# Optimization experiments

Hardware: AMD Instinct MI355X
Metric: run time of the kernel (lower is better)

Reference implementation:

```python
import jax, jax.numpy as jnp
import numpy as np

N_MFS = 2
N_FEATURES = 12
OUTPUT_DIM = 8
BATCH = 4096
N_RULES = N_MFS ** N_FEATURES  # 4096


def _rule_indices(n_features, n_mfs):
    r = np.arange(n_mfs ** n_features)
    # mixed-radix digits: indices[rule, feat] = (rule // n_mfs**feat) % n_mfs
    return np.stack([(r // (n_mfs ** f)) % n_mfs for f in range(n_features)], axis=1).astype(np.int32)


def setup_inputs() -> dict:
    key = jax.random.key(0)
    ks = jax.random.split(key, 6)
    x = jax.random.normal(ks[0], (BATCH, N_FEATURES), dtype=jnp.float32)
    center_base = jax.random.uniform(ks[1], (N_FEATURES, 1), minval=-1.0, maxval=0.0, dtype=jnp.float32)
    center_delta_raw = jax.random.normal(ks[2], (N_FEATURES, N_MFS - 1), dtype=jnp.float32) * 0.5
    width_raw = jax.random.normal(ks[3], (N_FEATURES, N_MFS), dtype=jnp.float32) * 0.5
    fan = N_RULES * N_FEATURES + OUTPUT_DIM
    limit = float(np.sqrt(6.0 / fan))
    consequent_p = jax.random.uniform(ks[4], (N_RULES, N_FEATURES, OUTPUT_DIM), minval=-limit, maxval=limit, dtype=jnp.float32)
    consequent_r = jnp.zeros((N_RULES, OUTPUT_DIM), dtype=jnp.float32)
    rule_mf_indices = jnp.asarray(_rule_indices(N_FEATURES, N_MFS))
    return {"x": x, "center_base": center_base, "center_delta_raw": center_delta_raw,
            "width_raw": width_raw, "consequent_p": consequent_p, "consequent_r": consequent_r,
            "rule_mf_indices": rule_mf_indices}


def reference(x, center_base, center_delta_raw, width_raw, consequent_p, consequent_r, rule_mf_indices):
    # ordered centers: base + cumsum(softplus(delta) + 1e-3)
    gaps = jax.nn.softplus(center_delta_raw) + 1e-3          # (F, M-1)
    offsets = jnp.cumsum(gaps, axis=1)
    centers = jnp.concatenate([center_base, center_base + offsets], axis=1)  # (F, M)
    widths = jax.nn.softplus(width_raw) + 1e-3                # (F, M)

    # Gaussian memberships: (B, F, M)
    d = x[:, :, None] - centers[None, :, :]
    memberships = jnp.exp(-jnp.square(d) / (2.0 * jnp.square(widths)[None, :, :]))

    # rule firing: product over features of gathered memberships (loop over small fixed F)
    firing = jnp.ones((x.shape[0], rule_mf_indices.shape[0]), dtype=x.dtype)  # (B, R)
    for f in range(memberships.shape[1]):
        firing = firing * memberships[:, f, :][:, rule_mf_indices[:, f]]
    firing_norm = firing / (jnp.sum(firing, axis=1, keepdims=True) + 1e-8)

    # per-rule linear consequents: (B, R, O)
    rule_outputs = jnp.einsum('bf,rfo->bro', x, consequent_p) + consequent_r[None, :, :]
    # weighted reduce over rules: (B, O)
    output = jnp.einsum('br,bro->bo', firing_norm, rule_outputs)
    return output
```

## Files before the change

### kernel.cpp

```cpp
#include <hip/hip_runtime.h>
#include <math.h>

#define NF 12
#define NB 4096
#define NR 4096
#define NO 8

typedef float f32x4v __attribute__((ext_vector_type(4)));
typedef short bf16x8 __attribute__((ext_vector_type(8)));
typedef unsigned int uint32x4 __attribute__((ext_vector_type(4)));

#define PT2_BYTES (128 * 8 * 512 * 2)
#define PPART_OFF PT2_BYTES
#define PPART_BYTES (8 * NB * NO * 4)
#define WS_NEED (PT2_BYTES + PPART_BYTES)
#define PT_ELEMS (112 * 4096)

__device__ __forceinline__ float softplus_f(float v) {
    return fmaxf(v, 0.0f) + log1pf(__expf(-fabsf(v)));
}
__device__ __forceinline__ unsigned short f2bf(float f) {
    unsigned u = __float_as_uint(f);
    u += 0x7FFFu + ((u >> 16) & 1u);
    return (unsigned short)(u >> 16);
}
__device__ __forceinline__ unsigned cvt_pk_bf16(float a, float b) {
    unsigned r;
    asm("v_cvt_pk_bf16_f32 %0, %1, %2" : "=v"(r) : "v"(a), "v"(b));
    return r;
}

__device__ __forceinline__ void build_split(f32x4v va, f32x4v vb,
                                            bf16x8& ah, bf16x8& al) {
    unsigned h0 = cvt_pk_bf16(va[0], va[1]), h1 = cvt_pk_bf16(va[2], va[3]);
    unsigned h2 = cvt_pk_bf16(vb[0], vb[1]), h3 = cvt_pk_bf16(vb[2], vb[3]);
    f32x4v hia = { __uint_as_float(h0 << 16), __uint_as_float(h0 & 0xFFFF0000u),
                   __uint_as_float(h1 << 16), __uint_as_float(h1 & 0xFFFF0000u) };
    f32x4v hib = { __uint_as_float(h2 << 16), __uint_as_float(h2 & 0xFFFF0000u),
                   __uint_as_float(h3 << 16), __uint_as_float(h3 & 0xFFFF0000u) };
    f32x4v ea = va - hia;
    f32x4v eb = vb - hib;
    unsigned q0 = cvt_pk_bf16(ea[0], ea[1]), q1 = cvt_pk_bf16(ea[2], ea[3]);
    unsigned q2 = cvt_pk_bf16(eb[0], eb[1]), q3 = cvt_pk_bf16(eb[2], eb[3]);
    union { uint32x4 u; bf16x8 v; } A, B;
    A.u = (uint32x4){h0, h1, h2, h3};
    B.u = (uint32x4){q0, q1, q2, q3};
    ah = A.v; al = B.v;
}

__global__ __launch_bounds__(512) void anfis_prep3(
    const float* __restrict__ cp, const float* __restrict__ cr,
    unsigned short* __restrict__ PT2)
{
    __shared__ float s_cp[32 * 97];
    __shared__ float s_cr[32 * 8];
    const int kt = blockIdx.x;
    const int tid = threadIdx.x;

    {
        const float4* cp4 = (const float4*)(cp + (size_t)kt * 32 * 96);
        for (int i = tid; i < 768; i += 512) {
            float4 v = cp4[i];
            int r = i / 24, c4 = i - r * 24;
            float* d = &s_cp[r * 97 + c4 * 4];
            d[0] = v.x; d[1] = v.y; d[2] = v.z; d[3] = v.w;
        }
        if (tid < 64) {
            float4 v = ((const float4*)(cr + (size_t)kt * 32 * 8))[tid];
            float* d = &s_cr[tid * 4];
            d[0] = v.x; d[1] = v.y; d[2] = v.z; d[3] = v.w;
        }
    }
    __syncthreads();

    const int g = tid >> 7, col = (tid >> 3) & 15, e = tid & 7;
    const int rr = g * 8 + e;
    #pragma unroll
    for (int j = 0; j < 8; ++j) {
        int n = j * 16 + col;
        float v = 0.f;
        if (n < 96) v = s_cp[rr * 97 + n];
        else if (n < 104) v = s_cr[rr * 8 + (n - 96)];
        PT2[(size_t)(kt * 8 + j) * 512 + tid] = f2bf(v);
    }
}

__global__ __launch_bounds__(512, 4) void anfis_main9(
    const float* __restrict__ x,
    const float* __restrict__ center_base, const float* __restrict__ cdr,
    const float* __restrict__ wr,
    const unsigned short* __restrict__ PT2,
    float* __restrict__ Ppart)
{
    __shared__ float s_params[48];
    __shared__ float s_x[64 * 12];
    __shared__ float s_low[64 * 36];
    __shared__ float s_highT[16 * 64];
    __shared__ __align__(16) unsigned char s_B[2 * 16384];

    const int tid = threadIdx.x;
    const int bid = blockIdx.x;
    const int ks = bid & 7;
    const int mt = bid >> 3;
    const int b0 = mt * 64;
    const int kt0 = ks * 16;

    const int w = tid >> 6, l = tid & 63;

    const unsigned char* ptBase = (const unsigned char*)PT2;
    #define STAGE(c, buf) do {                                                        \
        if (w != 7) {                                                                 \
            const unsigned char* gb = ptBase + ((size_t)(kt0 + 2 * (c)) << 13);       \
            unsigned char* lb = &s_B[(buf) * 16384];                                  \
            __builtin_amdgcn_global_load_lds(                                         \
                (const __attribute__((address_space(1))) void*)(gb + w * 1024 + l * 16),  \
                (__attribute__((address_space(3))) void*)(lb + w * 1024), 16, 0, 0);  \
            __builtin_amdgcn_global_load_lds(                                         \
                (const __attribute__((address_space(1))) void*)(gb + (8 + w) * 1024 + l * 16), \
                (__attribute__((address_space(3))) void*)(lb + (8 + w) * 1024), 16, 0, 0);\
        }                                                                             \
    } while (0)

    STAGE(0, 0);
    STAGE(1, 1);

    if (tid < 192) {
        float4 v = ((const float4*)(x + (size_t)b0 * NF))[tid];
        float* d = &s_x[tid * 4];
        d[0] = v.x; d[1] = v.y; d[2] = v.z; d[3] = v.w;
    }
    if (tid >= 500 && tid < 500 + NF) {
        int f = tid - 500;
        float c0 = center_base[f];
        float gap = softplus_f(cdr[f]) + 1e-3f;
        float w0 = softplus_f(wr[f * 2 + 0]) + 1e-3f;
        float w1 = softplus_f(wr[f * 2 + 1]) + 1e-3f;
        s_params[f * 4 + 0] = c0;
        s_params[f * 4 + 1] = c0 + gap;
        s_params[f * 4 + 2] = -0.5f / (w0 * w0);
        s_params[f * 4 + 3] = -0.5f / (w1 * w1);
    }
    __syncthreads();

    {
        const int row = tid >> 3, w8 = tid & 7;
        const float* xr = &s_x[row * 12];
        float m0a[NF], m1a[NF];
        float S = 1.f;
        #pragma unroll
        for (int f = 0; f < NF; ++f) {
            float4 pm = *(const float4*)&s_params[f * 4];
            float xv = xr[f];
            float d0 = xv - pm.x, d1 = xv - pm.y;
            float e0 = __expf(d0 * d0 * pm.z);
            float e1 = __expf(d1 * d1 * pm.w);
            m0a[f] = e0; m1a[f] = e1;
            S *= (e0 + e1);
        }
        float rc = 1.0f / (S + 1e-8f);
        #pragma unroll
        for (int i = 0; i < 4; ++i) {
            int ee = w8 * 4 + i;
            float p = 1.f;
            #pragma unroll
            for (int f = 0; f < 5; ++f)
                p *= ((ee >> f) & 1) ? m1a[f] : m0a[f];
            s_low[row * 36 + ee] = p;
        }
        #pragma unroll
        for (int i = 0; i < 2; ++i) {
            int t = w8 * 2 + i;
            int ktg = kt0 + t;
            float p = rc;
            #pragma unroll
            for (int ff = 0; ff < 7; ++ff)
                p *= ((ktg >> ff) & 1) ? m1a[5 + ff] : m0a[5 + ff];
            s_highT[t * 64 + row] = p;
        }
    }
    __syncthreads();

    const int rp = w >> 2, cq = w & 3;
    const int col = l & 15, g = l >> 4;
    const int nj = (cq < 3) ? 2 : 1;
    const int jb = cq * 2;

    bf16x8 ah[2], al[2];
    #pragma unroll
    for (int i = 0; i < 2; ++i) {
        int rowA = (rp * 2 + i) * 16 + col;
        f32x4v lo0 = *(const f32x4v*)&s_low[rowA * 36 + g * 8];
        f32x4v lo1 = *(const f32x4v*)&s_low[rowA * 36 + g * 8 + 4];
        build_split(lo0, lo1, ah[i], al[i]);
    }

    f32x4v acc[2][2];
    #pragma unroll
    for (int i = 0; i < 2; ++i)
        #pragma unroll
        for (int jj = 0; jj < 2; ++jj) acc[i][jj] = (f32x4v){0.f, 0.f, 0.f, 0.f};
    const f32x4v z4 = (f32x4v){0.f, 0.f, 0.f, 0.f};

    const int hoff0 = (rp * 2 + 0) * 16 + g * 4;
    const int hoff1 = (rp * 2 + 1) * 16 + g * 4;

    #pragma unroll 1
    for (int c = 0; c < 8; ++c) {
        const int cur = c & 1;
        if (c >= 1 && c + 1 < 8) STAGE(c + 1, cur ^ 1);
        #pragma unroll
        for (int kt2 = 0; kt2 < 2; ++kt2) {
            const int t = c * 2 + kt2;
            const unsigned char* base = &s_B[cur * 16384 + kt2 * 8192 + l * 16];
            bf16x8 fr0 = *(const bf16x8*)(base + jb * 1024);
            f32x4v hv0 = *(const f32x4v*)&s_highT[t * 64 + hoff0];
            f32x4v hv1 = *(const f32x4v*)&s_highT[t * 64 + hoff1];
            f32x4v q00, q10;
            q00 = __builtin_amdgcn_mfma_f32_16x16x32_bf16(ah[0], fr0, z4, 0, 0, 0);
            q00 = __builtin_amdgcn_mfma_f32_16x16x32_bf16(al[0], fr0, q00, 0, 0, 0);
            q10 = __builtin_amdgcn_mfma_f32_16x16x32_bf16(ah[1], fr0, z4, 0, 0, 0);
            q10 = __builtin_amdgcn_mfma_f32_16x16x32_bf16(al[1], fr0, q10, 0, 0, 0);
            acc[0][0] += hv0 * q00;
            acc[1][0] += hv1 * q10;
            if (nj == 2) {
                bf16x8 fr1 = *(const bf16x8*)(base + (jb + 1) * 1024);
                f32x4v q01, q11;
                q01 = __builtin_amdgcn_mfma_f32_16x16x32_bf16(ah[0], fr1, z4, 0, 0, 0);
                q01 = __builtin_amdgcn_mfma_f32_16x16x32_bf16(al[0], fr1, q01, 0, 0, 0);
                q11 = __builtin_amdgcn_mfma_f32_16x16x32_bf16(ah[1], fr1, z4, 0, 0, 0);
                q11 = __builtin_amdgcn_mfma_f32_16x16x32_bf16(al[1], fr1, q11, 0, 0, 0);
                acc[0][1] += hv0 * q01;
                acc[1][1] += hv1 * q11;
            }
        }
        __syncthreads();
    }
    #undef STAGE

    float* s_acc = (float*)s_B;
    #pragma unroll
    for (int i = 0; i < 2; ++i) {
        #pragma unroll
        for (int jj = 0; jj < 2; ++jj) {
            if (jj < nj) {
                int j = jb + jj;
                #pragma unroll
                for (int q = 0; q < 4; ++q)
                    s_acc[((rp * 2 + i) * 16 + g * 4 + q) * 116 + j * 16 + col] = acc[i][jj][q];
            }
        }
    }
    __syncthreads();
    {
        const int row = tid >> 3, o = tid & 7;
        const float* ar = &s_acc[row * 116];
        float t = ar[96 + o];
        #pragma unroll
        for (int f = 0; f < NF; ++f) t = fmaf(s_x[row * 12 + f], ar[f * 8 + o], t);
        Ppart[((size_t)ks * NB + b0 + row) * NO + o] = t;
    }
}

__global__ __launch_bounds__(256) void anfis_red2(
    const float* __restrict__ Ppart, float* __restrict__ out)
{
    const int i = blockIdx.x * 256 + threadIdx.x;
    const float4* p = (const float4*)Ppart;
    float4 a = p[i];
    #pragma unroll
    for (int ksi = 1; ksi < 8; ++ksi) {
        float4 b = p[(size_t)ksi * (NB * NO / 4) + i];
        a.x += b.x; a.y += b.y; a.z += b.z; a.w += b.w;
    }
    ((float4*)out)[i] = a;
}

__global__ __launch_bounds__(256) void anfis_prep(
    const float* __restrict__ cp, const float* __restrict__ cr,
    unsigned short* __restrict__ PT)
{
    const int n = blockIdx.x;
    const int t = threadIdx.x;
    if (n < 96) {
        #pragma unroll
        for (int i = 0; i < 16; ++i) { int r = i * 256 + t; PT[n * 4096 + r] = f2bf(cp[r * 96 + n]); }
    } else if (n < 104) {
        const int o = n - 96;
        #pragma unroll
        for (int i = 0; i < 16; ++i) { int r = i * 256 + t; PT[n * 4096 + r] = f2bf(cr[r * 8 + o]); }
    } else {
        #pragma unroll
        for (int i = 0; i < 16; ++i) PT[n * 4096 + i * 256 + t] = 0;
    }
}

__global__ __launch_bounds__(512) void anfis_mfma(
    const float* __restrict__ x,
    const float* __restrict__ center_base,
    const float* __restrict__ center_delta_raw,
    const float* __restrict__ width_raw,
    const unsigned short* __restrict__ PT,
    float* __restrict__ out)
{
    __shared__ float s_mem[16 * 26];
    __shared__ float s_low[16 * 36];
    __shared__ float s_high[16 * 132];
    __shared__ float s_red[8 * 16 * 113];

    const int tid = threadIdx.x;
    const int b0 = blockIdx.x * 16;

    if (tid < 16) {
        const int b = b0 + tid;
        float S = 1.0f;
        #pragma unroll
        for (int f = 0; f < NF; ++f) {
            float cb  = center_base[f];
            float gap = softplus_f(center_delta_raw[f]) + 1e-3f;
            float c0 = cb, c1 = cb + gap;
            float w0 = softplus_f(width_raw[f * 2 + 0]) + 1e-3f;
            float w1 = softplus_f(width_raw[f * 2 + 1]) + 1e-3f;
            float xv = x[b * NF + f];
            float d0 = xv - c0, d1 = xv - c1;
            float m0 = __expf(-d0 * d0 / (2.0f * w0 * w0));
            float m1 = __expf(-d1 * d1 / (2.0f * w1 * w1));
            s_mem[tid * 26 + f * 2 + 0] = m0;
            s_mem[tid * 26 + f * 2 + 1] = m1;
            S *= (m0 + m1);
        }
        s_mem[tid * 26 + 24] = 1.0f / (S + 1e-8f);
    }
    __syncthreads();
    if (tid < 256) {
        const int row = tid >> 4, w16 = tid & 15;
        const float* mrow = &s_mem[row * 26];
        #pragma unroll
        for (int e = 2 * w16; e <= 2 * w16 + 1; ++e) {
            float p = 1.0f;
            #pragma unroll
            for (int f = 0; f < 5; ++f) p *= mrow[f * 2 + ((e >> f) & 1)];
            s_low[row * 36 + e] = p;
        }
        float rcp = mrow[24];
        #pragma unroll
        for (int i = 0; i < 8; ++i) {
            int e = w16 + 16 * i;
            float p = rcp;
            #pragma unroll
            for (int ff = 0; ff < 7; ++ff) p *= mrow[(5 + ff) * 2 + ((e >> ff) & 1)];
            s_high[row * 132 + e] = p;
        }
    }
    __syncthreads();

    const int w = tid >> 6;
    const int l = tid & 63;
    const int col = l & 15;
    const int g   = l >> 4;

    f32x4v lo0 = *(const f32x4v*)&s_low[col * 36 + g * 8];
    f32x4v lo1 = *(const f32x4v*)&s_low[col * 36 + g * 8 + 4];
    f32x4v hq0 = *(const f32x4v*)&s_high[col * 132 + w * 16 + 0];
    f32x4v hq1 = *(const f32x4v*)&s_high[col * 132 + w * 16 + 4];
    f32x4v hq2 = *(const f32x4v*)&s_high[col * 132 + w * 16 + 8];
    f32x4v hq3 = *(const f32x4v*)&s_high[col * 132 + w * 16 + 12];

    const unsigned short* pB = PT + (size_t)col * 4096 + g * 8 + w * 512;

    f32x4v acc[7];
    #pragma unroll
    for (int j = 0; j < 7; ++j) acc[j] = (f32x4v){0.f, 0.f, 0.f, 0.f};

    bf16x8 bf[2][7];
    #pragma unroll
    for (int j = 0; j < 7; ++j) bf[0][j] = *(const bf16x8*)(pB + j * 65536 + 0 * 32);
    #pragma unroll
    for (int j = 0; j < 7; ++j) bf[1][j] = *(const bf16x8*)(pB + j * 65536 + 1 * 32);

    #pragma unroll
    for (int s = 0; s < 16; ++s) {
        const float hv = (s < 4) ? hq0[s & 3] : (s < 8) ? hq1[s & 3]
                        : (s < 12) ? hq2[s & 3] : hq3[s & 3];
        bf16x8 ah, al;
        #pragma unroll
        for (int e = 0; e < 8; ++e) {
            float v = ((e < 4) ? lo0[e & 3] : lo1[e & 3]) * hv;
            unsigned short h = f2bf(v);
            float vh = __uint_as_float(((unsigned)h) << 16);
            ah[e] = (short)h;
            al[e] = (short)f2bf(v - vh);
        }
        #pragma unroll
        for (int j = 0; j < 7; ++j) {
            acc[j] = __builtin_amdgcn_mfma_f32_16x16x32_bf16(ah, bf[s & 1][j], acc[j], 0, 0, 0);
            acc[j] = __builtin_amdgcn_mfma_f32_16x16x32_bf16(al, bf[s & 1][j], acc[j], 0, 0, 0);
        }
        if (s + 2 < 16) {
            #pragma unroll
            for (int j = 0; j < 7; ++j)
                bf[s & 1][j] = *(const bf16x8*)(pB + j * 65536 + (s + 2) * 32);
        }
    }

    #pragma unroll
    for (int j = 0; j < 7; ++j)
        #pragma unroll
        for (int q = 0; q < 4; ++q)
            s_red[(w * 16 + g * 4 + q) * 113 + j * 16 + col] = acc[j][q];
    __syncthreads();

    if (tid < 128) {
        const int row = tid >> 3, o = tid & 7;
        float xr[NF];
        #pragma unroll
        for (int f = 0; f < NF; ++f) xr[f] = x[(b0 + row) * NF + f];
        float outv = 0.0f;
        #pragma unroll
        for (int ww = 0; ww < 8; ++ww) {
            const float* ar = &s_red[(ww * 16 + row) * 113];
            float t2 = ar[96 + o];
            #pragma unroll
            for (int f = 0; f < NF; ++f) t2 = fmaf(xr[f], ar[f * 8 + o], t2);
            outv += t2;
        }
        out[(b0 + row) * NO + o] = outv;
    }
}

extern "C" void kernel_launch(void* const* d_in, const int* in_sizes, int n_in,
                              void* d_out, int out_size, void* d_ws, size_t ws_size,
                              hipStream_t stream) {
    const float* x   = (const float*)d_in[0];
    const float* cb  = (const float*)d_in[1];
    const float* cdr = (const float*)d_in[2];
    const float* wr  = (const float*)d_in[3];
    const float* cp  = (const float*)d_in[4];
    const float* cr  = (const float*)d_in[5];
    float* out = (float*)d_out;

    if (ws_size >= (size_t)WS_NEED) {
        unsigned short* PT2 = (unsigned short*)d_ws;
        float* Ppart = (float*)((char*)d_ws + PPART_OFF);
        anfis_prep3<<<128, 512, 0, stream>>>(cp, cr, PT2);
        anfis_main9<<<512, 512, 0, stream>>>(x, cb, cdr, wr, PT2, Ppart);
        anfis_red2<<<NB * NO / 4 / 256, 256, 0, stream>>>(Ppart, out);
    } else if (ws_size >= (size_t)PT_ELEMS * sizeof(unsigned short)) {
        unsigned short* PT = (unsigned short*)d_ws;
        anfis_prep<<<112, 256, 0, stream>>>(cp, cr, PT);
        anfis_mfma<<<NB / 16, 512, 0, stream>>>(x, cb, cdr, wr, PT, out);
    }
}
```

Before: 24.49 us.

## Replace split-K reduction kernel with atomics and load B fragments directly from global

Removes the separate reduction kernel: the prep kernel now zeroes the output and the main kernel atomically adds its split-K partial results into it, which drops one launch and the partial-buffer round trip. The main loop no longer stages PT2 tiles into LDS with double buffering. Each wave reads its bf16 fragments straight from global memory, and the waves split the K range into two halves whose results are merged in LDS. Each wave now covers all 64 rows (4 A fragments), raising register use. Direct global loads may expose more latency, and float atomics make the summation order nondeterministic.

New measurement: 81.76 us. +233.8%, slower.

```diff
diff --git a/kernel.cpp b/kernel.cpp
--- a/kernel.cpp
+++ b/kernel.cpp
@@ -11,9 +11,7 @@
 typedef unsigned int uint32x4 __attribute__((ext_vector_type(4)));
 
 #define PT2_BYTES (128 * 8 * 512 * 2)
-#define PPART_OFF PT2_BYTES
-#define PPART_BYTES (8 * NB * NO * 4)
-#define WS_NEED (PT2_BYTES + PPART_BYTES)
+#define WS_NEED (PT2_BYTES + 2048)
 #define PT_ELEMS (112 * 4096)
 
 __device__ __forceinline__ float softplus_f(float v) {
@@ -48,14 +46,16 @@
     ah = A.v; al = B.v;
 }
 
-__global__ __launch_bounds__(512) void anfis_prep3(
+__global__ __launch_bounds__(512) void anfis_prep4(
     const float* __restrict__ cp, const float* __restrict__ cr,
-    unsigned short* __restrict__ PT2)
+    unsigned short* __restrict__ PT2, float* __restrict__ out_zero)
 {
     __shared__ float s_cp[32 * 97];
     __shared__ float s_cr[32 * 8];
     const int kt = blockIdx.x;
     const int tid = threadIdx.x;
+
+    if (kt < 64) out_zero[(size_t)kt * 512 + tid] = 0.0f;
 
     {
         const float4* cp4 = (const float4*)(cp + (size_t)kt * 32 * 96);
@@ -85,18 +85,18 @@
     }
 }
 
-__global__ __launch_bounds__(512, 4) void anfis_main9(
+__global__ __launch_bounds__(512, 4) void anfis_main10(
     const float* __restrict__ x,
     const float* __restrict__ center_base, const float* __restrict__ cdr,
     const float* __restrict__ wr,
     const unsigned short* __restrict__ PT2,
-    float* __restrict__ Ppart)
+    float* __restrict__ out)
 {
     __shared__ float s_params[48];
     __shared__ float s_x[64 * 12];
     __shared__ float s_low[64 * 36];
     __shared__ float s_highT[16 * 64];
-    __shared__ __align__(16) unsigned char s_B[2 * 16384];
+    __shared__ __align__(16) float s_acc[64 * 116];
 
     const int tid = threadIdx.x;
     const int bid = blockIdx.x;
@@ -106,23 +106,6 @@
     const int kt0 = ks * 16;
 
     const int w = tid >> 6, l = tid & 63;
-
-    const unsigned char* ptBase = (const unsigned char*)PT2;
-    #define STAGE(c, buf) do {                                                        \
-        if (w != 7) {                                                                 \
-            const unsigned char* gb = ptBase + ((size_t)(kt0 + 2 * (c)) << 13);       \
-            unsigned char* lb = &s_B[(buf) * 16384];                                  \
-            __builtin_amdgcn_global_load_lds(                                         \
-                (const __attribute__((address_space(1))) void*)(gb + w * 1024 + l * 16),  \
-                (__attribute__((address_space(3))) void*)(lb + w * 1024), 16, 0, 0);  \
-            __builtin_amdgcn_global_load_lds(                                         \
-                (const __attribute__((address_space(1))) void*)(gb + (8 + w) * 1024 + l * 16), \
-                (__attribute__((address_space(3))) void*)(lb + (8 + w) * 1024), 16, 0, 0);\
-        }                                                                             \
-    } while (0)
-
-    STAGE(0, 0);
-    STAGE(1, 1);
 
     if (tid < 192) {
         float4 v = ((const float4*)(x + (size_t)b0 * NF))[tid];
@@ -180,75 +163,82 @@
     }
     __syncthreads();
 
-    const int rp = w >> 2, cq = w & 3;
+    const int h = w >> 2, cq = w & 3;
     const int col = l & 15, g = l >> 4;
     const int nj = (cq < 3) ? 2 : 1;
     const int jb = cq * 2;
 
-    bf16x8 ah[2], al[2];
-    #pragma unroll
-    for (int i = 0; i < 2; ++i) {
-        int rowA = (rp * 2 + i) * 16 + col;
+    bf16x8 ah[4], al[4];
+    #pragma unroll
+    for (int i = 0; i < 4; ++i) {
+        int rowA = i * 16 + col;
         f32x4v lo0 = *(const f32x4v*)&s_low[rowA * 36 + g * 8];
         f32x4v lo1 = *(const f32x4v*)&s_low[rowA * 36 + g * 8 + 4];
         build_split(lo0, lo1, ah[i], al[i]);
     }
 
-    f32x4v acc[2][2];
-    #pragma unroll
-    for (int i = 0; i < 2; ++i)
+    f32x4v acc[4][2];
+    #pragma unroll
+    for (int i = 0; i < 4; ++i)
         #pragma unroll
         for (int jj = 0; jj < 2; ++jj) acc[i][jj] = (f32x4v){0.f, 0.f, 0.f, 0.f};
     const f32x4v z4 = (f32x4v){0.f, 0.f, 0.f, 0.f};
 
-    const int hoff0 = (rp * 2 + 0) * 16 + g * 4;
-    const int hoff1 = (rp * 2 + 1) * 16 + g * 4;
-
-    #pragma unroll 1
-    for (int c = 0; c < 8; ++c) {
-        const int cur = c & 1;
-        if (c >= 1 && c + 1 < 8) STAGE(c + 1, cur ^ 1);
-        #pragma unroll
-        for (int kt2 = 0; kt2 < 2; ++kt2) {
-            const int t = c * 2 + kt2;
-            const unsigned char* base = &s_B[cur * 16384 + kt2 * 8192 + l * 16];
-            bf16x8 fr0 = *(const bf16x8*)(base + jb * 1024);
-            f32x4v hv0 = *(const f32x4v*)&s_highT[t * 64 + hoff0];
-            f32x4v hv1 = *(const f32x4v*)&s_highT[t * 64 + hoff1];
-            f32x4v q00, q10;
-            q00 = __builtin_amdgcn_mfma_f32_16x16x32_bf16(ah[0], fr0, z4, 0, 0, 0);
-            q00 = __builtin_amdgcn_mfma_f32_16x16x32_bf16(al[0], fr0, q00, 0, 0, 0);
-            q10 = __builtin_amdgcn_mfma_f32_16x16x32_bf16(ah[1], fr0, z4, 0, 0, 0);
-            q10 = __builtin_amdgcn_mfma_f32_16x16x32_bf16(al[1], fr0, q10, 0, 0, 0);
-            acc[0][0] += hv0 * q00;
-            acc[1][0] += hv1 * q10;
-            if (nj == 2) {
-                bf16x8 fr1 = *(const bf16x8*)(base + (jb + 1) * 1024);
-                f32x4v q01, q11;
-                q01 = __builtin_amdgcn_mfma_f32_16x16x32_bf16(ah[0], fr1, z4, 0, 0, 0);
-                q01 = __builtin_amdgcn_mfma_f32_16x16x32_bf16(al[0], fr1, q01, 0, 0, 0);
-                q11 = __builtin_amdgcn_mfma_f32_16x16x32_bf16(ah[1], fr1, z4, 0, 0, 0);
-                q11 = __builtin_amdgcn_mfma_f32_16x16x32_bf16(al[1], fr1, q11, 0, 0, 0);
-                acc[0][1] += hv0 * q01;
-                acc[1][1] += hv1 * q11;
-            }
-        }
-        __syncthreads();
-    }
-    #undef STAGE
-
-    float* s_acc = (float*)s_B;
-    #pragma unroll
-    for (int i = 0; i < 2; ++i) {
+    const unsigned char* pB = (const unsigned char*)PT2
+                            + ((size_t)(kt0 + h * 8) << 13) + (size_t)l * 16;
+
+    #pragma unroll
+    for (int tt = 0; tt < 8; ++tt) {
+        const int t = h * 8 + tt;
+        f32x4v hv0 = *(const f32x4v*)&s_highT[t * 64 +  0 + g * 4];
+        f32x4v hv1 = *(const f32x4v*)&s_highT[t * 64 + 16 + g * 4];
+        f32x4v hv2 = *(const f32x4v*)&s_highT[t * 64 + 32 + g * 4];
+        f32x4v hv3 = *(const f32x4v*)&s_highT[t * 64 + 48 + g * 4];
         #pragma unroll
         for (int jj = 0; jj < 2; ++jj) {
             if (jj < nj) {
-                int j = jb + jj;
-                #pragma unroll
-                for (int q = 0; q < 4; ++q)
-                    s_acc[((rp * 2 + i) * 16 + g * 4 + q) * 116 + j * 16 + col] = acc[i][jj][q];
+                bf16x8 fr = *(const bf16x8*)(pB + tt * 8192 + (jb + jj) * 1024);
+                f32x4v q0, q1, q2, q3;
+                q0 = __builtin_amdgcn_mfma_f32_16x16x32_bf16(ah[0], fr, z4, 0, 0, 0);
+                q1 = __builtin_amdgcn_mfma_f32_16x16x32_bf16(ah[1], fr, z4, 0, 0, 0);
+                q2 = __builtin_amdgcn_mfma_f32_16x16x32_bf16(ah[2], fr, z4, 0, 0, 0);
+                q3 = __builtin_amdgcn_mfma_f32_16x16x32_bf16(ah[3], fr, z4, 0, 0, 0);
+                q0 = __builtin_amdgcn_mfma_f32_16x16x32_bf16(al[0], fr, q0, 0, 0, 0);
+                q1 = __builtin_amdgcn_mfma_f32_16x16x32_bf16(al[1], fr, q1, 0, 0, 0);
+                q2 = __builtin_amdgcn_mfma_f32_16x16x32_bf16(al[2], fr, q2, 0, 0, 0);
+                q3 = __builtin_amdgcn_mfma_f32_16x16x32_bf16(al[3], fr, q3, 0, 0, 0);
+                acc[0][jj] += hv0 * q0;
+                acc[1][jj] += hv1 * q1;
+                acc[2][jj] += hv2 * q2;
+                acc[3][jj] += hv3 * q3;
             }
         }
+    }
+
+    if (h == 0) {
+        #pragma unroll
+        for (int i = 0; i < 4; ++i)
+            #pragma unroll
+            for (int jj = 0; jj < 2; ++jj)
+                if (jj < nj) {
+                    int j = jb + jj;
+                    #pragma unroll
+                    for (int q = 0; q < 4; ++q)
+                        s_acc[(i * 16 + g * 4 + q) * 116 + j * 16 + col] = acc[i][jj][q];
+                }
+    }
+    __syncthreads();
+    if (h == 1) {
+        #pragma unroll
+        for (int i = 0; i < 4; ++i)
+            #pragma unroll
+            for (int jj = 0; jj < 2; ++jj)
+                if (jj < nj) {
+                    int j = jb + jj;
+                    #pragma unroll
+                    for (int q = 0; q < 4; ++q)
+                        s_acc[(i * 16 + g * 4 + q) * 116 + j * 16 + col] += acc[i][jj][q];
+                }
     }
     __syncthreads();
     {
@@ -257,22 +247,8 @@
         float t = ar[96 + o];
         #pragma unroll
         for (int f = 0; f < NF; ++f) t = fmaf(s_x[row * 12 + f], ar[f * 8 + o], t);
-        Ppart[((size_t)ks * NB + b0 + row) * NO + o] = t;
-    }
-}
-
-__global__ __launch_bounds__(256) void anfis_red2(
-    const float* __restrict__ Ppart, float* __restrict__ out)
-{
-    const int i = blockIdx.x * 256 + threadIdx.x;
-    const float4* p = (const float4*)Ppart;
-    float4 a = p[i];
-    #pragma unroll
-    for (int ksi = 1; ksi < 8; ++ksi) {
-        float4 b = p[(size_t)ksi * (NB * NO / 4) + i];
-        a.x += b.x; a.y += b.y; a.z += b.z; a.w += b.w;
-    }
-    ((float4*)out)[i] = a;
+        atomicAdd(&out[(size_t)(b0 + row) * NO + o], t);
+    }
 }
 
 __global__ __launch_bounds__(256) void anfis_prep(
@@ -440,10 +416,8 @@
 
     if (ws_size >= (size_t)WS_NEED) {
         unsigned short* PT2 = (unsigned short*)d_ws;
-        float* Ppart = (float*)((char*)d_ws + PPART_OFF);
-        anfis_prep3<<<128, 512, 0, stream>>>(cp, cr, PT2);
-        anfis_main9<<<512, 512, 0, stream>>>(x, cb, cdr, wr, PT2, Ppart);
-        anfis_red2<<<NB * NO / 4 / 256, 256, 0, stream>>>(Ppart, out);
+        anfis_prep4<<<128, 512, 0, stream>>>(cp, cr, PT2, out);
+        anfis_main10<<<512, 512, 0, stream>>>(x, cb, cdr, wr, PT2, out);
     } else if (ws_size >= (size_t)PT_ELEMS * sizeof(unsigned short)) {
         unsigned short* PT = (unsigned short*)d_ws;
         anfis_prep<<<112, 256, 0, stream>>>(cp, cr, PT);
```
